# Kernel tuning notes

Hardware: AMD Instinct MI355X
Metric: run time of the kernel (lower is better)

## Reference

```python
import jax, jax.numpy as jnp
import numpy as np

TEMPERATURE = 2.0
SOFT_LAMBDA = 0.5
SMOOTH_L1_BETA = 1.0  # CFG.smooth_l1_beta (torch default)
EPS_COS = 1e-8
EPS_LOG = 1e-7


def _offdiag(x):
    # x: [n, n] -> [n, n-1], dropping the diagonal, preserving column order.
    n = x.shape[0]
    cols = jnp.arange(n - 1)
    idx = cols[None, :] + (cols[None, :] >= jnp.arange(n)[:, None])
    return x[jnp.arange(n)[:, None], idx]


def _cos_pair_diff(v):
    # 1 - pairwise cosine similarity, norms clamped at eps (torch CosineSimilarity).
    nv = jnp.maximum(jnp.linalg.norm(v, axis=-1), EPS_COS)
    cos = (v @ v.T) / (nv[:, None] * nv[None, :])
    return 1.0 - cos


def setup_inputs() -> dict:
    key = jax.random.key(0)
    k1, k2, k3, k4, k5 = jax.random.split(key, 5)
    n, d_feat = 384, 128
    return {
        "trans_feat": jax.random.normal(k1, (n, d_feat), dtype=jnp.float32),
        "rot_green": jax.random.normal(k2, (n, 3), dtype=jnp.float32),
        "rot_red": jax.random.normal(k3, (n, 3), dtype=jnp.float32),
        "trans": jax.random.normal(k4, (n, 3), dtype=jnp.float32),
        "sym": jax.random.randint(k5, (n, 1), 0, 2, dtype=jnp.int32),
    }


def reference(trans_feat, rot_green, rot_red, trans, sym):
    n = trans_feat.shape[0]

    # ---- label differences ----
    # trans: smooth-L1 over pairwise diffs, mean over coord dim -> [n, n]
    d = trans[:, None, :] - trans[None, :, :]
    ad = jnp.abs(d)
    sl1 = jnp.where(ad < SMOOTH_L1_BETA, 0.5 * d * d / SMOOTH_L1_BETA, ad - 0.5 * SMOOTH_L1_BETA)
    trans_diff = sl1.mean(-1)

    g = _cos_pair_diff(rot_green)
    r = _cos_pair_diff(rot_red)
    sym_mask = sym[:, 0] == 1
    pair_sym = sym_mask[:, None] | sym_mask[None, :]
    rot_diff = jnp.where(pair_sym, g, g + r)

    # ---- feature similarity logits (negative L2, zero-safe norm) ----
    fd = trans_feat[:, None, :] - trans_feat[None, :, :]
    sq = jnp.sum(fd * fd, axis=-1)
    norm = jnp.where(sq > 0, jnp.sqrt(jnp.where(sq > 0, sq, 1.0)), 0.0)
    logits = -norm / TEMPERATURE
    logits = logits - jnp.max(logits, axis=1, keepdims=True)
    exp_logits = jnp.exp(logits)

    lo = _offdiag(logits)      # [n, n-1]
    eo = _offdiag(exp_logits)  # [n, n-1]
    td = _offdiag(trans_diff)  # [n, n-1]
    rd = _offdiag(rot_diff)    # [n, n-1]

    # rank masks: mask[i, j, k] = diff[i, j] <= diff[i, k]
    trans_mask = td[:, :, None] <= td[:, None, :]
    hard_mask = trans_mask & (rd[:, :, None] <= rd[:, None, :])

    den_trans = jnp.einsum('ijk,ik->ij', trans_mask.astype(lo.dtype), eo)
    den_hard = jnp.einsum('ijk,ik->ij', hard_mask.astype(lo.dtype), eo)

    pos_trans = lo - jnp.log(den_trans + EPS_LOG)
    pos_hard = lo - jnp.log(den_hard + EPS_LOG)

    denom = n * (n - 1)
    loss_hard = -jnp.sum(pos_hard) / denom
    loss_trans = -jnp.sum(pos_trans) / denom
    return loss_hard + SOFT_LAMBDA * loss_trans
```

## Files before the change

### kernel.cpp

```cpp
#include <hip/hip_runtime.h>
#include <math.h>

#define N 384
#define DF 128
#define TI 16
#define TK 16
#define TEMP 2.0f
#define SOFT_LAMBDA 0.5f
#define BETA 1.0f
#define EPS_COS 1e-8f
#define EPS_LOG 1e-7f

__global__ __launch_bounds__(256) void rnc_pairs(
    const float* __restrict__ feat,
    const float* __restrict__ rg,
    const float* __restrict__ rr,
    const float* __restrict__ tr,
    const int*   __restrict__ sym,
    float4* __restrict__ pk,
    float* __restrict__ out)
{
    const int i0 = blockIdx.y * TI;
    const int k0 = blockIdx.x * TK;
    const int t = threadIdx.x;

    __shared__ __align__(16) float4 fi_s[TI][DF / 4 + 1];
    __shared__ __align__(16) float4 fk_s[TK][DF / 4 + 1];
    __shared__ float4 hi_s[TI], gi_s[TI], ri_s[TI];
    __shared__ float4 hk_s[TK], gk_s[TK], rk_s[TK];

    if (blockIdx.x == 0 && blockIdx.y == 0 && t == 0) out[0] = 0.f;

    if (t < TI) {
        int g = i0 + t;
        hi_s[t] = make_float4(tr[g * 3], tr[g * 3 + 1], tr[g * 3 + 2],
                              (sym[g] == 1) ? 1.f : 0.f);
        float a = rg[g * 3], b = rg[g * 3 + 1], c = rg[g * 3 + 2];
        gi_s[t] = make_float4(a, b, c, fmaxf(sqrtf(a * a + b * b + c * c), EPS_COS));
        float d = rr[g * 3], e = rr[g * 3 + 1], f = rr[g * 3 + 2];
        ri_s[t] = make_float4(d, e, f, fmaxf(sqrtf(d * d + e * e + f * f), EPS_COS));
    } else if (t >= 32 && t < 32 + TK) {
        int g = k0 + (t - 32);
        int tl = t - 32;
        hk_s[tl] = make_float4(tr[g * 3], tr[g * 3 + 1], tr[g * 3 + 2],
                               (sym[g] == 1) ? 1.f : 0.f);
        float a = rg[g * 3], b = rg[g * 3 + 1], c = rg[g * 3 + 2];
        gk_s[tl] = make_float4(a, b, c, fmaxf(sqrtf(a * a + b * b + c * c), EPS_COS));
        float d = rr[g * 3], e = rr[g * 3 + 1], f = rr[g * 3 + 2];
        rk_s[tl] = make_float4(d, e, f, fmaxf(sqrtf(d * d + e * e + f * f), EPS_COS));
    }

    const float4* feat4 = reinterpret_cast<const float4*>(feat);
#pragma unroll
    for (int idx = 0; idx < 2; ++idx) {
        int u = t + idx * 256;
        int row = u >> 5, c = u & 31;
        fi_s[row][c] = feat4[(i0 + row) * (DF / 4) + c];
        fk_s[row][c] = feat4[(k0 + row) * (DF / 4) + c];
    }
    __syncthreads();

    const int ii = t >> 4, kk = t & 15;
    float sq = 0.f;
#pragma unroll
    for (int d = 0; d < DF / 4; ++d) {
        float4 a = fi_s[ii][d];
        float4 b = fk_s[kk][d];
        float dx = a.x - b.x, dy = a.y - b.y, dz = a.z - b.z, dw = a.w - b.w;
        sq += dx * dx + dy * dy + dz * dz + dw * dw;
    }
    const int gi = i0 + ii, gk = k0 + kk;
    float dist = (sq > 0.f) ? sqrtf(sq) : 0.f;
    float lo = -dist * (1.0f / TEMP);
    float eo = (gi == gk) ? 0.f : expf(lo);

    float4 ha = hi_s[ii], hb = hk_s[kk];
    float d0 = ha.x - hb.x, d1 = ha.y - hb.y, d2 = ha.z - hb.z;
    float a0 = fabsf(d0), a1 = fabsf(d1), a2 = fabsf(d2);
    float s = ((a0 < BETA) ? (0.5f * d0 * d0 / BETA) : (a0 - 0.5f * BETA))
            + ((a1 < BETA) ? (0.5f * d1 * d1 / BETA) : (a1 - 0.5f * BETA))
            + ((a2 < BETA) ? (0.5f * d2 * d2 / BETA) : (a2 - 0.5f * BETA));
    float td = s * (1.0f / 3.0f);

    float4 ga = gi_s[ii], gb = gk_s[kk];
    float gdiff = 1.0f - (ga.x * gb.x + ga.y * gb.y + ga.z * gb.z) / (ga.w * gb.w);
    float4 ra = ri_s[ii], rb = rk_s[kk];
    float rdiff = 1.0f - (ra.x * rb.x + ra.y * rb.y + ra.z * rb.z) / (ra.w * rb.w);
    bool pair_sym = (ha.w != 0.f) || (hb.w != 0.f);
    float rd = pair_sym ? gdiff : (gdiff + rdiff);

    pk[gi * N + gk] = make_float4(td, rd, eo, lo);
}

__global__ __launch_bounds__(512) void rnc_rank(
    const float4* __restrict__ pk,
    float* __restrict__ out)
{
    const int i = blockIdx.x;
    const int t = threadIdx.x;

    __shared__ __align__(16) float4 pks[N];
    __shared__ float dpt[8][N];
    __shared__ float dph[8][N];
    __shared__ float red_h[8], red_t[8];

    if (t < N) pks[t] = pk[i * N + t];
    __syncthreads();

    const int w = t >> 6, l = t & 63;
    const int jb = l * 6;
    float tdj[6], rdj[6];
    float dent[6] = {0.f, 0.f, 0.f, 0.f, 0.f, 0.f};
    float denh[6] = {0.f, 0.f, 0.f, 0.f, 0.f, 0.f};
#pragma unroll
    for (int jj = 0; jj < 6; ++jj) {
        float4 p = pks[jb + jj];
        tdj[jj] = p.x;
        rdj[jj] = p.y;
    }
    const int k0 = w * 48;
#pragma unroll 4
    for (int k = k0; k < k0 + 48; ++k) {
        float4 p = pks[k];
#pragma unroll
        for (int jj = 0; jj < 6; ++jj) {
            bool mt = p.x >= tdj[jj];
            bool mh = mt && (p.y >= rdj[jj]);
            dent[jj] += mt ? p.z : 0.f;
            denh[jj] += mh ? p.z : 0.f;
        }
    }
#pragma unroll
    for (int jj = 0; jj < 6; ++jj) {
        dpt[w][jb + jj] = dent[jj];
        dph[w][jb + jj] = denh[jj];
    }
    __syncthreads();

    float pos_h = 0.f, pos_t = 0.f;
    if (t < N && t != i) {
        float st_ = 0.f, sh_ = 0.f;
#pragma unroll
        for (int g = 0; g < 8; ++g) {
            st_ += dpt[g][t];
            sh_ += dph[g][t];
        }
        float lo = pks[t].w;
        pos_h = lo - logf(sh_ + EPS_LOG);
        pos_t = lo - logf(st_ + EPS_LOG);
    }
#pragma unroll
    for (int off = 32; off > 0; off >>= 1) {
        pos_h += __shfl_down(pos_h, off, 64);
        pos_t += __shfl_down(pos_t, off, 64);
    }
    if (l == 0) {
        red_h[w] = pos_h;
        red_t[w] = pos_t;
    }
    __syncthreads();
    if (t == 0) {
        float sh = 0.f, st = 0.f;
#pragma unroll
        for (int g = 0; g < 8; ++g) {
            sh += red_h[g];
            st += red_t[g];
        }
        const float scale = -1.0f / ((float)N * (float)(N - 1));
        atomicAdd(out, (sh + SOFT_LAMBDA * st) * scale);
    }
}

extern "C" void kernel_launch(void* const* d_in, const int* in_sizes, int n_in,
                              void* d_out, int out_size, void* d_ws, size_t ws_size,
                              hipStream_t stream) {
    const float* feat = (const float*)d_in[0];
    const float* rg   = (const float*)d_in[1];
    const float* rr   = (const float*)d_in[2];
    const float* tr   = (const float*)d_in[3];
    const int*   sym  = (const int*)d_in[4];
    float* out = (float*)d_out;

    float4* pk = (float4*)d_ws;

    dim3 gridA(N / TK, N / TI);
    rnc_pairs<<<gridA, 256, 0, stream>>>(feat, rg, rr, tr, sym, pk, out);
    rnc_rank<<<N, 512, 0, stream>>>(pk, out);
}
```

Baseline: 81.67 us.

## Split packed pair data into SoA planes and halve rank work per block

The pair kernel now writes td/rd/eo/lo to four separate planes instead of one interleaved float4 array. The rank kernel reads these as float4 vectors of four consecutive k values, and each row is split across two blocks (2N blocks) that each handle 192 j columns. This is meant to raise parallelism and cut shared-memory load traffic per compare. In exchange the k-sweep and staging loads are repeated in both blocks, and the pair kernel now issues scalar strided stores.

```diff
diff --git a/kernel.cpp b/kernel.cpp
--- a/kernel.cpp
+++ b/kernel.cpp
@@ -17,7 +17,10 @@
     const float* __restrict__ rr,
     const float* __restrict__ tr,
     const int*   __restrict__ sym,
-    float4* __restrict__ pk,
+    float* __restrict__ ptd,
+    float* __restrict__ prd,
+    float* __restrict__ peo,
+    float* __restrict__ plo,
     float* __restrict__ out)
 {
     const int i0 = blockIdx.y * TI;
@@ -89,65 +92,100 @@
     bool pair_sym = (ha.w != 0.f) || (hb.w != 0.f);
     float rd = pair_sym ? gdiff : (gdiff + rdiff);
 
-    pk[gi * N + gk] = make_float4(td, rd, eo, lo);
+    const int idx = gi * N + gk;
+    ptd[idx] = td;
+    prd[idx] = rd;
+    peo[idx] = eo;
+    plo[idx] = lo;
 }
 
 __global__ __launch_bounds__(512) void rnc_rank(
-    const float4* __restrict__ pk,
+    const float* __restrict__ ptd,
+    const float* __restrict__ prd,
+    const float* __restrict__ peo,
+    const float* __restrict__ plo,
     float* __restrict__ out)
 {
-    const int i = blockIdx.x;
+    const int i = blockIdx.x >> 1;
+    const int h = blockIdx.x & 1;
     const int t = threadIdx.x;
 
-    __shared__ __align__(16) float4 pks[N];
-    __shared__ float dpt[8][N];
-    __shared__ float dph[8][N];
+    __shared__ __align__(16) float td_s[N];
+    __shared__ __align__(16) float rd_s[N];
+    __shared__ __align__(16) float eo_s[N];
+    __shared__ float dpt[8][192];
+    __shared__ float dph[8][192];
     __shared__ float red_h[8], red_t[8];
 
-    if (t < N) pks[t] = pk[i * N + t];
+    if (t < 96) {
+        reinterpret_cast<float4*>(td_s)[t] =
+            reinterpret_cast<const float4*>(ptd + i * N)[t];
+    } else if (t < 192) {
+        reinterpret_cast<float4*>(rd_s)[t - 96] =
+            reinterpret_cast<const float4*>(prd + i * N)[t - 96];
+    } else if (t < 288) {
+        reinterpret_cast<float4*>(eo_s)[t - 192] =
+            reinterpret_cast<const float4*>(peo + i * N)[t - 192];
+    }
     __syncthreads();
 
     const int w = t >> 6, l = t & 63;
-    const int jb = l * 6;
-    float tdj[6], rdj[6];
-    float dent[6] = {0.f, 0.f, 0.f, 0.f, 0.f, 0.f};
-    float denh[6] = {0.f, 0.f, 0.f, 0.f, 0.f, 0.f};
-#pragma unroll
-    for (int jj = 0; jj < 6; ++jj) {
-        float4 p = pks[jb + jj];
-        tdj[jj] = p.x;
-        rdj[jj] = p.y;
-    }
-    const int k0 = w * 48;
+    const int jl = l * 3;
+    float tdj[3], rdj[3];
+    float dent[3] = {0.f, 0.f, 0.f};
+    float denh[3] = {0.f, 0.f, 0.f};
+#pragma unroll
+    for (int jj = 0; jj < 3; ++jj) {
+        tdj[jj] = td_s[h * 192 + jl + jj];
+        rdj[jj] = rd_s[h * 192 + jl + jj];
+    }
+
+    const float4* td4 = reinterpret_cast<const float4*>(td_s);
+    const float4* rd4 = reinterpret_cast<const float4*>(rd_s);
+    const float4* eo4 = reinterpret_cast<const float4*>(eo_s);
+    const int k4b = w * 12;
 #pragma unroll 4
-    for (int k = k0; k < k0 + 48; ++k) {
-        float4 p = pks[k];
-#pragma unroll
-        for (int jj = 0; jj < 6; ++jj) {
-            bool mt = p.x >= tdj[jj];
-            bool mh = mt && (p.y >= rdj[jj]);
-            dent[jj] += mt ? p.z : 0.f;
-            denh[jj] += mh ? p.z : 0.f;
+    for (int k4 = k4b; k4 < k4b + 12; ++k4) {
+        float4 tv = td4[k4];
+        float4 rv = rd4[k4];
+        float4 ev = eo4[k4];
+#pragma unroll
+        for (int jj = 0; jj < 3; ++jj) {
+            bool m0 = tv.x >= tdj[jj];
+            bool m1 = tv.y >= tdj[jj];
+            bool m2 = tv.z >= tdj[jj];
+            bool m3 = tv.w >= tdj[jj];
+            dent[jj] += m0 ? ev.x : 0.f;
+            dent[jj] += m1 ? ev.y : 0.f;
+            dent[jj] += m2 ? ev.z : 0.f;
+            dent[jj] += m3 ? ev.w : 0.f;
+            denh[jj] += (m0 && rv.x >= rdj[jj]) ? ev.x : 0.f;
+            denh[jj] += (m1 && rv.y >= rdj[jj]) ? ev.y : 0.f;
+            denh[jj] += (m2 && rv.z >= rdj[jj]) ? ev.z : 0.f;
+            denh[jj] += (m3 && rv.w >= rdj[jj]) ? ev.w : 0.f;
         }
     }
 #pragma unroll
-    for (int jj = 0; jj < 6; ++jj) {
-        dpt[w][jb + jj] = dent[jj];
-        dph[w][jb + jj] = denh[jj];
+    for (int jj = 0; jj < 3; ++jj) {
+        dpt[w][jl + jj] = dent[jj];
+        dph[w][jl + jj] = denh[jj];
     }
     __syncthreads();
 
     float pos_h = 0.f, pos_t = 0.f;
-    if (t < N && t != i) {
-        float st_ = 0.f, sh_ = 0.f;
-#pragma unroll
-        for (int g = 0; g < 8; ++g) {
-            st_ += dpt[g][t];
-            sh_ += dph[g][t];
+    if (t < 192) {
+        const int j = h * 192 + t;
+        if (j != i) {
+            float st_ = 0.f, sh_ = 0.f;
+#pragma unroll
+            for (int g = 0; g < 8; ++g) {
+                st_ += dpt[g][t];
+                sh_ += dph[g][t];
+            }
+            float lo = plo[i * N + j];
+            pos_h = lo - logf(sh_ + EPS_LOG);
+            pos_t = lo - logf(st_ + EPS_LOG);
         }
-        float lo = pks[t].w;
-        pos_h = lo - logf(sh_ + EPS_LOG);
-        pos_t = lo - logf(st_ + EPS_LOG);
     }
 #pragma unroll
     for (int off = 32; off > 0; off >>= 1) {
@@ -181,9 +219,12 @@
     const int*   sym  = (const int*)d_in[4];
     float* out = (float*)d_out;
 
-    float4* pk = (float4*)d_ws;
+    float* ptd = (float*)d_ws;
+    float* prd = ptd + (size_t)N * N;
+    float* peo = prd + (size_t)N * N;
+    float* plo = peo + (size_t)N * N;
 
     dim3 gridA(N / TK, N / TI);
-    rnc_pairs<<<gridA, 256, 0, stream>>>(feat, rg, rr, tr, sym, pk, out);
-    rnc_rank<<<N, 512, 0, stream>>>(pk, out);
+    rnc_pairs<<<gridA, 256, 0, stream>>>(feat, rg, rr, tr, sym, ptd, prd, peo, plo, out);
+    rnc_rank<<<2 * N, 512, 0, stream>>>(ptd, prd, peo, plo, out);
 }
```

Result: no change. 82.92 us (+1.5%).
